# Kernel tuning notes

Hardware: AMD Instinct MI355X
Metric: run time of the kernel (lower is better)

Reference implementation:

```python
import jax, jax.numpy as jnp
import numpy as np

TEMPERATURE = 10.0
CE_WEIGHT = 10.0
NUM_CLUSTERS = 32  # clusters per batch element, labels in [0, K)


def setup_inputs() -> dict:
    key = jax.random.key(0)
    k1, k2, k3, k4, k5 = jax.random.split(key, 5)
    B, N, D, C, K = 4, 2048, 2, 64, NUM_CLUSTERS
    embedding = jax.random.normal(k1, (B, N, D), dtype=jnp.float32)
    contr_emb = jax.random.normal(k2, (B, N, C), dtype=jnp.float32)
    abs_coords = jax.random.normal(k3, (B, N, D), dtype=jnp.float32)
    patch_mask = jax.random.randint(k4, (B, N, N), 0, 2, dtype=jnp.int32)
    cluster_labels = jax.random.randint(k5, (B, N), 0, K, dtype=jnp.int32)
    return {
        "embedding": embedding,
        "contr_emb": contr_emb,
        "abs_coords": abs_coords,
        "patch_mask": patch_mask,
        "cluster_labels": cluster_labels,
    }


def reference(embedding, contr_emb, abs_coords, patch_mask, cluster_labels):
    B, N, D = embedding.shape
    C = contr_emb.shape[-1]
    K = NUM_CLUSTERS

    # --- anchor term: pairwise distance + nonlinearity + masked mean ---
    # diff[b,i,j,:] = (e_i - e_j) + (c_i - c_j)
    diff = (embedding[:, :, None] - embedding[:, None]) + (
        abs_coords[:, :, None] - abs_coords[:, None]
    )  # [B,N,N,D]
    dist_sq = jnp.sum(diff * diff, axis=-1)  # norm(2)^2, [B,N,N]
    nonlinear_dist = 1.0 - jnp.exp(-dist_sq / TEMPERATURE)
    m = (patch_mask == 1).astype(nonlinear_dist.dtype)
    loss = jnp.sum(nonlinear_dist * m) / jnp.sum(m)  # masked mean

    # --- contrastive term ---
    # F.normalize(contr_emb, dim=-1)
    norm = jnp.maximum(jnp.linalg.norm(contr_emb, axis=-1, keepdims=True), 1e-12)
    c = contr_emb / norm  # [B,N,C]

    # per-batch cluster means under no_grad (stop_gradient)
    onehot = jax.nn.one_hot(cluster_labels, K, dtype=c.dtype)  # [B,N,K]
    sums = jnp.einsum("bnc,bnk->bkc", c, onehot)  # [B,K,C]
    counts = jnp.maximum(jnp.sum(onehot, axis=1), 1.0)  # [B,K]
    means = jax.lax.stop_gradient(sums / counts[..., None])  # [B,K,C]

    # cat per-batch [C,K] matrices along cluster axis -> [C, B*K]
    cum_mean_clusters = means.reshape(B * K, C).T
    stacked = c.reshape(B * N, C)
    logits = stacked @ cum_mean_clusters  # [B*N, B*K]

    target = cluster_labels.reshape(-1)  # labels as written (no batch offset)
    logp = jax.nn.log_softmax(logits, axis=-1)
    nll = -jnp.take_along_axis(logp, target[:, None].astype(jnp.int32), axis=1)[:, 0]
    bce_loss = jnp.mean(nll)  # all targets >= 0, so no ignore_index hits

    return loss + CE_WEIGHT * bce_loss
```

## Files before the change

kernel.cpp:

```cpp
#include <hip/hip_runtime.h>
#include <math.h>

#define B_ 4
#define N_ 2048
#define C_ 64
#define K_ 32
#define BN_ (B_ * N_)

#define WS_NLL 0
#define WS_DONE 8
#define WS_MEANS 64
#define WS_APART 8320
#define WS_SX 10432
#define WS_SY 18624

__device__ __forceinline__ void proc4(int4 m, float rx, float ry,
                                      float4 xs, float4 ys,
                                      float& S, int& cnt) {
  float dx, dy, d2;
  dx = rx - xs.x; dy = ry - ys.x; d2 = dx * dx + dy * dy;
  S += (float)m.x * __expf(d2 * -0.1f); cnt += m.x;
  dx = rx - xs.y; dy = ry - ys.y; d2 = dx * dx + dy * dy;
  S += (float)m.y * __expf(d2 * -0.1f); cnt += m.y;
  dx = rx - xs.z; dy = ry - ys.z; d2 = dx * dx + dy * dy;
  S += (float)m.z * __expf(d2 * -0.1f); cnt += m.z;
  dx = rx - xs.w; dy = ry - ys.w; d2 = dx * dx + dy * dy;
  S += (float)m.w * __expf(d2 * -0.1f); cnt += m.w;
}

__global__ __launch_bounds__(256) void k_cluster(
    const float* __restrict__ emb, const float* __restrict__ absc,
    const float* __restrict__ contr, const int* __restrict__ labels,
    float* __restrict__ ws) {
  __shared__ int lab[N_];
  __shared__ float lsum[4][64];
  __shared__ float lcnt[4];
  int t = threadIdx.x, lane = t & 63, w = t >> 6;
  int bid = blockIdx.x;
  int b = bid >> 5, k = bid & 31;
  if (bid == 0 && t == 0) {
    ws[WS_NLL] = 0.0f;
    ((unsigned*)ws)[WS_DONE] = 0u;
  }
  int flat = bid * 256 + t;
  if (flat < BN_) {
    float2 ev = ((const float2*)emb)[flat];
    float2 av = ((const float2*)absc)[flat];
    ws[WS_SX + flat] = ev.x + av.x;
    ws[WS_SY + flat] = ev.y + av.y;
  }
  const int4* lab4 = (const int4*)(labels + b * N_);
  int4* l4 = (int4*)lab;
  l4[t] = lab4[t];
  l4[t + 256] = lab4[t + 256];
  __syncthreads();
  float acc = 0.0f, cnt = 0.0f;
  for (int g0 = w * 512; g0 < w * 512 + 512; g0 += 64) {
    unsigned long long mb = __ballot(lab[g0 + lane] == k);
    while (mb) {
      int bit = __ffsll(mb) - 1;
      mb &= mb - 1;
      int r = g0 + bit;
      float x = contr[(size_t)(b * N_ + r) * C_ + lane];
      float ss = x * x;
#pragma unroll
      for (int off = 32; off > 0; off >>= 1) ss += __shfl_xor(ss, off);
      acc += x * (1.0f / fmaxf(sqrtf(ss), 1e-12f));
      cnt += 1.0f;
    }
  }
  lsum[w][lane] = acc;
  if (lane == 0) lcnt[w] = cnt;
  __syncthreads();
  if (t < 64) {
    float s = lsum[0][t] + lsum[1][t] + lsum[2][t] + lsum[3][t];
    float c = lcnt[0] + lcnt[1] + lcnt[2] + lcnt[3];
    ws[WS_MEANS + (b * K_ + k) * C_ + t] = s / fmaxf(c, 1.0f);
  }
}

__global__ __launch_bounds__(256) void k_fused(
    const float* __restrict__ contr, const int* __restrict__ labels,
    const int* __restrict__ mask, float* __restrict__ ws,
    float* __restrict__ out) {
  __shared__ float lc[32 * C_];
  __shared__ float invr[32];
  __shared__ float lsv[2][32], ltl[32];
  __shared__ float red[8];
  __shared__ float fred[8];
  __shared__ int lastf;
  int t = threadIdx.x, lane = t & 63, w = t >> 6;
  int bid = blockIdx.x;
  if (bid < 256) {
    int r0 = bid * 32;
    int ch = w & 1, rh = w >> 1;
    int j = ch * 64 + lane;
    const float4* mean4 = (const float4*)(ws + WS_MEANS);
    float4 mk[16];
#pragma unroll
    for (int q = 0; q < 16; ++q) mk[q] = mean4[j * 16 + q];
    const float4* c4 = (const float4*)(contr + (size_t)r0 * C_);
    float4* lc4 = (float4*)lc;
    lc4[t] = c4[t];
    lc4[t + 256] = c4[t + 256];
    __syncthreads();
    if (t < 32) {
      float ss = 0.0f;
#pragma unroll
      for (int q = 0; q < 16; ++q) {
        float4 v = lc4[t * 16 + q];
        ss += v.x * v.x + v.y * v.y + v.z * v.z + v.w * v.w;
      }
      invr[t] = 1.0f / fmaxf(sqrtf(ss), 1e-12f);
    }
    __syncthreads();
#pragma unroll 1
    for (int rg = 0; rg < 4; ++rg) {
      int rb = rh * 16 + rg * 4;
      const float4* cr = lc4 + rb * 16;
      float a0 = 0.0f, a1 = 0.0f, a2 = 0.0f, a3 = 0.0f;
#pragma unroll
      for (int q = 0; q < 16; ++q) {
        float4 m = mk[q];
        float4 c0 = cr[q], c1 = cr[16 + q], c2 = cr[32 + q], c3 = cr[48 + q];
        a0 += c0.x * m.x + c0.y * m.y + c0.z * m.z + c0.w * m.w;
        a1 += c1.x * m.x + c1.y * m.y + c1.z * m.z + c1.w * m.w;
        a2 += c2.x * m.x + c2.y * m.y + c2.z * m.z + c2.w * m.w;
        a3 += c3.x * m.x + c3.y * m.y + c3.z * m.z + c3.w * m.w;
      }
      float l0 = a0 * invr[rb + 0];
      float l1 = a1 * invr[rb + 1];
      float l2 = a2 * invr[rb + 2];
      float l3 = a3 * invr[rb + 3];
      float s0 = __expf(l0), s1 = __expf(l1), s2 = __expf(l2), s3 = __expf(l3);
#pragma unroll
      for (int off = 32; off > 0; off >>= 1) {
        s0 += __shfl_xor(s0, off);
        s1 += __shfl_xor(s1, off);
        s2 += __shfl_xor(s2, off);
        s3 += __shfl_xor(s3, off);
      }
      int tg0 = labels[r0 + rb + 0], tg1 = labels[r0 + rb + 1];
      int tg2 = labels[r0 + rb + 2], tg3 = labels[r0 + rb + 3];
      float t0 = __shfl(l0, tg0), t1 = __shfl(l1, tg1);
      float t2 = __shfl(l2, tg2), t3 = __shfl(l3, tg3);
      if (lane == 0) {
        lsv[ch][rb + 0] = s0; lsv[ch][rb + 1] = s1;
        lsv[ch][rb + 2] = s2; lsv[ch][rb + 3] = s3;
        if (ch == 0) { ltl[rb] = t0; ltl[rb + 1] = t1; ltl[rb + 2] = t2; ltl[rb + 3] = t3; }
      }
    }
    __syncthreads();
    if (t < 32) {
      float nll = __logf(lsv[0][t] + lsv[1][t]) - ltl[t];
#pragma unroll
      for (int off = 16; off > 0; off >>= 1) nll += __shfl_xor(nll, off);
      if (t == 0) atomicAdd(&ws[WS_NLL], nll);
    }
  } else {
    int aid = bid - 256;
    int b = aid >> 8;
    int aid8 = aid & 255;
    const float* sxp = ws + WS_SX + b * N_;
    const float* syp = ws + WS_SY + b * N_;
    int cg = (aid8 & 1) * 256 + t;
    float4 xs = ((const float4*)sxp)[cg];
    float4 ys = ((const float4*)syp)[cg];
    int rb0 = aid8 >> 1;
    const int4* mp = (const int4*)mask + (size_t)b * (N_ * (size_t)N_ / 4)
                     + aid8 * 256 + t;
    int4 c0 = mp[0], c1 = mp[65536], c2 = mp[131072], c3 = mp[196608];
    float S = 0.0f;
    int cnt = 0;
#pragma unroll 1
    for (int g = 0; g < 3; ++g) {
      const int4* np = mp + (size_t)(g + 1) * 262144;
      int4 n0 = np[0], n1 = np[65536], n2 = np[131072], n3 = np[196608];
      int rr = rb0 + g * 512;
      proc4(c0, sxp[rr],       syp[rr],       xs, ys, S, cnt);
      proc4(c1, sxp[rr + 128], syp[rr + 128], xs, ys, S, cnt);
      proc4(c2, sxp[rr + 256], syp[rr + 256], xs, ys, S, cnt);
      proc4(c3, sxp[rr + 384], syp[rr + 384], xs, ys, S, cnt);
      c0 = n0; c1 = n1; c2 = n2; c3 = n3;
    }
    int rr = rb0 + 3 * 512;
    proc4(c0, sxp[rr],       syp[rr],       xs, ys, S, cnt);
    proc4(c1, sxp[rr + 128], syp[rr + 128], xs, ys, S, cnt);
    proc4(c2, sxp[rr + 256], syp[rr + 256], xs, ys, S, cnt);
    proc4(c3, sxp[rr + 384], syp[rr + 384], xs, ys, S, cnt);
    float cntf = (float)cnt;
    float acc = cntf - S;
#pragma unroll
    for (int off = 32; off > 0; off >>= 1) {
      acc += __shfl_xor(acc, off);
      cntf += __shfl_xor(cntf, off);
    }
    if (lane == 0) { red[w * 2] = acc; red[w * 2 + 1] = cntf; }
    __syncthreads();
    if (t == 0) {
      ws[WS_APART + aid * 2 + 0] = red[0] + red[2] + red[4] + red[6];
      ws[WS_APART + aid * 2 + 1] = red[1] + red[3] + red[5] + red[7];
    }
  }
  __syncthreads();
  if (t == 0) {
    __threadfence();
    unsigned v = atomicAdd(&((unsigned*)ws)[WS_DONE], 1u);
    lastf = (v == 1279u);
  }
  __syncthreads();
  if (lastf) {
    __threadfence();
    float a = 0.0f, c = 0.0f;
    for (int i = t; i < 1024; i += 256) {
      a += ws[WS_APART + i * 2 + 0];
      c += ws[WS_APART + i * 2 + 1];
    }
#pragma unroll
    for (int off = 32; off > 0; off >>= 1) {
      a += __shfl_xor(a, off);
      c += __shfl_xor(c, off);
    }
    if (lane == 0) { fred[w * 2] = a; fred[w * 2 + 1] = c; }
    __syncthreads();
    if (t == 0) {
      float at = fred[0] + fred[2] + fred[4] + fred[6];
      float ct = fred[1] + fred[3] + fred[5] + fred[7];
      out[0] = at / ct + 10.0f * ws[WS_NLL] * (1.0f / (float)BN_);
    }
  }
}

extern "C" void kernel_launch(void* const* d_in, const int* in_sizes, int n_in,
                              void* d_out, int out_size, void* d_ws, size_t ws_size,
                              hipStream_t stream) {
  const float* emb    = (const float*)d_in[0];
  const float* contr  = (const float*)d_in[1];
  const float* absc   = (const float*)d_in[2];
  const int*   mask   = (const int*)d_in[3];
  const int*   labels = (const int*)d_in[4];
  float* ws  = (float*)d_ws;
  float* out = (float*)d_out;

  k_cluster<<<B_ * K_, 256, 0, stream>>>(emb, absc, contr, labels, ws);
  k_fused<<<256 + 1024, 256, 0, stream>>>(contr, labels, mask, ws, out);
}
```

Before: 156.0 us.

## Compute anchor coordinate sums in LDS per block and reorder block roles

The anchor blocks now load embedding and abs_coords straight into shared memory and sum them there. This replaces reading precomputed sums from the workspace, which k_cluster used to write. The anchor blocks are also given the low block indices so the mask-streaming work is scheduled first, and the row-norm computation in the logit blocks is spread across all warps with shuffles. The catch is that every anchor block reloads 32 KB of coordinates, and the union grows shared memory per block to 16 KB.

```diff
diff --git a/kernel.cpp b/kernel.cpp
--- a/kernel.cpp
+++ b/kernel.cpp
@@ -11,8 +11,6 @@
 #define WS_DONE 8
 #define WS_MEANS 64
 #define WS_APART 8320
-#define WS_SX 10432
-#define WS_SY 18624
 
 __device__ __forceinline__ void proc4(int4 m, float rx, float ry,
                                       float4 xs, float4 ys,
@@ -29,7 +27,6 @@
 }
 
 __global__ __launch_bounds__(256) void k_cluster(
-    const float* __restrict__ emb, const float* __restrict__ absc,
     const float* __restrict__ contr, const int* __restrict__ labels,
     float* __restrict__ ws) {
   __shared__ int lab[N_];
@@ -42,13 +39,6 @@
     ws[WS_NLL] = 0.0f;
     ((unsigned*)ws)[WS_DONE] = 0u;
   }
-  int flat = bid * 256 + t;
-  if (flat < BN_) {
-    float2 ev = ((const float2*)emb)[flat];
-    float2 av = ((const float2*)absc)[flat];
-    ws[WS_SX + flat] = ev.x + av.x;
-    ws[WS_SY + flat] = ev.y + av.y;
-  }
   const int4* lab4 = (const int4*)(labels + b * N_);
   int4* l4 = (int4*)lab;
   l4[t] = lab4[t];
@@ -80,19 +70,75 @@
 }
 
 __global__ __launch_bounds__(256) void k_fused(
+    const float* __restrict__ emb, const float* __restrict__ absc,
     const float* __restrict__ contr, const int* __restrict__ labels,
     const int* __restrict__ mask, float* __restrict__ ws,
     float* __restrict__ out) {
-  __shared__ float lc[32 * C_];
-  __shared__ float invr[32];
-  __shared__ float lsv[2][32], ltl[32];
+  __shared__ union {
+    struct { float sx[N_]; float sy[N_]; } a;
+    struct { float lc[32 * C_]; float invr[32];
+             float lsv[2][32]; float ltl[32]; } l;
+  } sm;
   __shared__ float red[8];
   __shared__ float fred[8];
   __shared__ int lastf;
   int t = threadIdx.x, lane = t & 63, w = t >> 6;
   int bid = blockIdx.x;
-  if (bid < 256) {
-    int r0 = bid * 32;
+  if (bid < 1024) {
+    int aid = bid;
+    int b = aid >> 8;
+    int aid8 = aid & 255;
+    const float4* e4 = (const float4*)(emb + b * N_ * 2);
+    const float4* a4 = (const float4*)(absc + b * N_ * 2);
+    for (int i = t; i < N_ / 2; i += 256) {
+      float4 ev = e4[i], av = a4[i];
+      sm.a.sx[2 * i]     = ev.x + av.x;
+      sm.a.sy[2 * i]     = ev.y + av.y;
+      sm.a.sx[2 * i + 1] = ev.z + av.z;
+      sm.a.sy[2 * i + 1] = ev.w + av.w;
+    }
+    __syncthreads();
+    int cg = (aid8 & 1) * 256 + t;
+    float4 xs = ((const float4*)sm.a.sx)[cg];
+    float4 ys = ((const float4*)sm.a.sy)[cg];
+    int rb0 = aid8 >> 1;
+    const int4* mp = (const int4*)mask + (size_t)b * (N_ * (size_t)N_ / 4)
+                     + aid8 * 256 + t;
+    int4 c0 = mp[0], c1 = mp[65536], c2 = mp[131072], c3 = mp[196608];
+    float S = 0.0f;
+    int cnt = 0;
+#pragma unroll 1
+    for (int g = 0; g < 3; ++g) {
+      const int4* np = mp + (size_t)(g + 1) * 262144;
+      int4 n0 = np[0], n1 = np[65536], n2 = np[131072], n3 = np[196608];
+      int rr = rb0 + g * 512;
+      proc4(c0, sm.a.sx[rr],       sm.a.sy[rr],       xs, ys, S, cnt);
+      proc4(c1, sm.a.sx[rr + 128], sm.a.sy[rr + 128], xs, ys, S, cnt);
+      proc4(c2, sm.a.sx[rr + 256], sm.a.sy[rr + 256], xs, ys, S, cnt);
+      proc4(c3, sm.a.sx[rr + 384], sm.a.sy[rr + 384], xs, ys, S, cnt);
+      c0 = n0; c1 = n1; c2 = n2; c3 = n3;
+    }
+    int rr = rb0 + 3 * 512;
+    proc4(c0, sm.a.sx[rr],       sm.a.sy[rr],       xs, ys, S, cnt);
+    proc4(c1, sm.a.sx[rr + 128], sm.a.sy[rr + 128], xs, ys, S, cnt);
+    proc4(c2, sm.a.sx[rr + 256], sm.a.sy[rr + 256], xs, ys, S, cnt);
+    proc4(c3, sm.a.sx[rr + 384], sm.a.sy[rr + 384], xs, ys, S, cnt);
+    float cntf = (float)cnt;
+    float acc = cntf - S;
+#pragma unroll
+    for (int off = 32; off > 0; off >>= 1) {
+      acc += __shfl_xor(acc, off);
+      cntf += __shfl_xor(cntf, off);
+    }
+    if (lane == 0) { red[w * 2] = acc; red[w * 2 + 1] = cntf; }
+    __syncthreads();
+    if (t == 0) {
+      ws[WS_APART + aid * 2 + 0] = red[0] + red[2] + red[4] + red[6];
+      ws[WS_APART + aid * 2 + 1] = red[1] + red[3] + red[5] + red[7];
+    }
+  } else {
+    int lid = bid - 1024;
+    int r0 = lid * 32;
     int ch = w & 1, rh = w >> 1;
     int j = ch * 64 + lane;
     const float4* mean4 = (const float4*)(ws + WS_MEANS);
@@ -100,18 +146,16 @@
 #pragma unroll
     for (int q = 0; q < 16; ++q) mk[q] = mean4[j * 16 + q];
     const float4* c4 = (const float4*)(contr + (size_t)r0 * C_);
-    float4* lc4 = (float4*)lc;
+    float4* lc4 = (float4*)sm.l.lc;
     lc4[t] = c4[t];
     lc4[t + 256] = c4[t + 256];
     __syncthreads();
-    if (t < 32) {
-      float ss = 0.0f;
-#pragma unroll
-      for (int q = 0; q < 16; ++q) {
-        float4 v = lc4[t * 16 + q];
-        ss += v.x * v.x + v.y * v.y + v.z * v.z + v.w * v.w;
-      }
-      invr[t] = 1.0f / fmaxf(sqrtf(ss), 1e-12f);
+    for (int r = w * 8; r < w * 8 + 8; ++r) {
+      float x = sm.l.lc[r * C_ + lane];
+      float ss = x * x;
+#pragma unroll
+      for (int off = 32; off > 0; off >>= 1) ss += __shfl_xor(ss, off);
+      if (lane == 0) sm.l.invr[r] = 1.0f / fmaxf(sqrtf(ss), 1e-12f);
     }
     __syncthreads();
 #pragma unroll 1
@@ -128,10 +172,10 @@
         a2 += c2.x * m.x + c2.y * m.y + c2.z * m.z + c2.w * m.w;
         a3 += c3.x * m.x + c3.y * m.y + c3.z * m.z + c3.w * m.w;
       }
-      float l0 = a0 * invr[rb + 0];
-      float l1 = a1 * invr[rb + 1];
-      float l2 = a2 * invr[rb + 2];
-      float l3 = a3 * invr[rb + 3];
+      float l0 = a0 * sm.l.invr[rb + 0];
+      float l1 = a1 * sm.l.invr[rb + 1];
+      float l2 = a2 * sm.l.invr[rb + 2];
+      float l3 = a3 * sm.l.invr[rb + 3];
       float s0 = __expf(l0), s1 = __expf(l1), s2 = __expf(l2), s3 = __expf(l3);
 #pragma unroll
       for (int off = 32; off > 0; off >>= 1) {
@@ -145,61 +189,20 @@
       float t0 = __shfl(l0, tg0), t1 = __shfl(l1, tg1);
       float t2 = __shfl(l2, tg2), t3 = __shfl(l3, tg3);
       if (lane == 0) {
-        lsv[ch][rb + 0] = s0; lsv[ch][rb + 1] = s1;
-        lsv[ch][rb + 2] = s2; lsv[ch][rb + 3] = s3;
-        if (ch == 0) { ltl[rb] = t0; ltl[rb + 1] = t1; ltl[rb + 2] = t2; ltl[rb + 3] = t3; }
+        sm.l.lsv[ch][rb + 0] = s0; sm.l.lsv[ch][rb + 1] = s1;
+        sm.l.lsv[ch][rb + 2] = s2; sm.l.lsv[ch][rb + 3] = s3;
+        if (ch == 0) {
+          sm.l.ltl[rb + 0] = t0; sm.l.ltl[rb + 1] = t1;
+          sm.l.ltl[rb + 2] = t2; sm.l.ltl[rb + 3] = t3;
+        }
       }
     }
     __syncthreads();
     if (t < 32) {
-      float nll = __logf(lsv[0][t] + lsv[1][t]) - ltl[t];
+      float nll = __logf(sm.l.lsv[0][t] + sm.l.lsv[1][t]) - sm.l.ltl[t];
 #pragma unroll
       for (int off = 16; off > 0; off >>= 1) nll += __shfl_xor(nll, off);
       if (t == 0) atomicAdd(&ws[WS_NLL], nll);
-    }
-  } else {
-    int aid = bid - 256;
-    int b = aid >> 8;
-    int aid8 = aid & 255;
-    const float* sxp = ws + WS_SX + b * N_;
-    const float* syp = ws + WS_SY + b * N_;
-    int cg = (aid8 & 1) * 256 + t;
-    float4 xs = ((const float4*)sxp)[cg];
-    float4 ys = ((const float4*)syp)[cg];
-    int rb0 = aid8 >> 1;
-    const int4* mp = (const int4*)mask + (size_t)b * (N_ * (size_t)N_ / 4)
-                     + aid8 * 256 + t;
-    int4 c0 = mp[0], c1 = mp[65536], c2 = mp[131072], c3 = mp[196608];
-    float S = 0.0f;
-    int cnt = 0;
-#pragma unroll 1
-    for (int g = 0; g < 3; ++g) {
-      const int4* np = mp + (size_t)(g + 1) * 262144;
-      int4 n0 = np[0], n1 = np[65536], n2 = np[131072], n3 = np[196608];
-      int rr = rb0 + g * 512;
-      proc4(c0, sxp[rr],       syp[rr],       xs, ys, S, cnt);
-      proc4(c1, sxp[rr + 128], syp[rr + 128], xs, ys, S, cnt);
-      proc4(c2, sxp[rr + 256], syp[rr + 256], xs, ys, S, cnt);
-      proc4(c3, sxp[rr + 384], syp[rr + 384], xs, ys, S, cnt);
-      c0 = n0; c1 = n1; c2 = n2; c3 = n3;
-    }
-    int rr = rb0 + 3 * 512;
-    proc4(c0, sxp[rr],       syp[rr],       xs, ys, S, cnt);
-    proc4(c1, sxp[rr + 128], syp[rr + 128], xs, ys, S, cnt);
-    proc4(c2, sxp[rr + 256], syp[rr + 256], xs, ys, S, cnt);
-    proc4(c3, sxp[rr + 384], syp[rr + 384], xs, ys, S, cnt);
-    float cntf = (float)cnt;
-    float acc = cntf - S;
-#pragma unroll
-    for (int off = 32; off > 0; off >>= 1) {
-      acc += __shfl_xor(acc, off);
-      cntf += __shfl_xor(cntf, off);
-    }
-    if (lane == 0) { red[w * 2] = acc; red[w * 2 + 1] = cntf; }
-    __syncthreads();
-    if (t == 0) {
-      ws[WS_APART + aid * 2 + 0] = red[0] + red[2] + red[4] + red[6];
-      ws[WS_APART + aid * 2 + 1] = red[1] + red[3] + red[5] + red[7];
     }
   }
   __syncthreads();
@@ -242,6 +245,6 @@
   float* ws  = (float*)d_ws;
   float* out = (float*)d_out;
 
-  k_cluster<<<B_ * K_, 256, 0, stream>>>(emb, absc, contr, labels, ws);
-  k_fused<<<256 + 1024, 256, 0, stream>>>(contr, labels, mask, ws, out);
-}
+  k_cluster<<<B_ * K_, 256, 0, stream>>>(contr, labels, ws);
+  k_fused<<<1024 + 256, 256, 0, stream>>>(emb, absc, contr, labels, mask, ws, out);
+}
```

New measurement: 172.3 us. +10.4%, slower.
